# Performance work log

Hardware: AMD Instinct MI355X
Metric: run time of the kernel (lower is better)

Reference implementation:

```python
import jax, jax.numpy as jnp
import numpy as np

EMBED = 1024
HEADS = 16
HEAD_DIM = EMBED // HEADS


def setup_inputs() -> dict:
    key = jax.random.key(0)
    ks = jax.random.split(key, 7)
    N, S = 2, 2048
    k = jax.random.normal(ks[0], (N, S, EMBED), dtype=jnp.float32)
    q = jax.random.normal(ks[1], (N, S, EMBED), dtype=jnp.float32)
    v = jax.random.normal(ks[2], (N, S, EMBED), dtype=jnp.float32)
    sc = 1.0 / np.sqrt(HEAD_DIM)
    # nn.Linear weights, applied as x @ W.T
    Wk = jax.random.normal(ks[3], (HEAD_DIM, HEAD_DIM), dtype=jnp.float32) * sc
    Wq = jax.random.normal(ks[4], (HEAD_DIM, HEAD_DIM), dtype=jnp.float32) * sc
    Wv = jax.random.normal(ks[5], (HEAD_DIM, HEAD_DIM), dtype=jnp.float32) * sc
    Wo = jax.random.normal(ks[6], (EMBED, EMBED), dtype=jnp.float32) / np.sqrt(EMBED)
    return {"k": k, "q": q, "v": v, "Wk": Wk, "Wq": Wq, "Wv": Wv, "Wo": Wo}


def reference(k, q, v, Wk, Wq, Wv, Wo):
    N, S, _ = q.shape
    # reshape to [N, S, H, D]; per-head projection weights shared across heads
    kh = jnp.einsum('nshd,ed->nshe', k.reshape(N, S, HEADS, HEAD_DIM), Wk)
    qh = jnp.einsum('nshd,ed->nshe', q.reshape(N, S, HEADS, HEAD_DIM), Wq)
    vh = jnp.einsum('nshd,ed->nshe', v.reshape(N, S, HEADS, HEAD_DIM), Wv)
    # energy: [N, H, q_len, k_len]
    energy = jnp.einsum('nqhd,nkhd->nhqk', qh, kh)
    attn = jax.nn.softmax(energy / jnp.sqrt(jnp.float32(HEAD_DIM)), axis=-1)
    out = jnp.einsum('nhqk,nkhd->nqhd', attn, vh).reshape(N, S, EMBED)
    return out @ Wo.T
```

## Files before the change

kernel.cpp:

```cpp
#include <hip/hip_runtime.h>

#define SQ   2048
#define HEADS 16
#define HD   64
#define EMB  1024

typedef __attribute__((ext_vector_type(2))) __fp16 h2;
typedef __attribute__((ext_vector_type(4))) __fp16 h4;
typedef __attribute__((ext_vector_type(8))) __fp16 h8;
typedef __attribute__((ext_vector_type(4))) float f4;
typedef unsigned short USH;
typedef unsigned int   UI;

__device__ __forceinline__ UI pkh(float a, float b) {
    h2 v = __builtin_amdgcn_cvt_pkrtz(a, b);
    return __builtin_bit_cast(UI, v);
}

__device__ __forceinline__ void glds16(const void* g, void* l) {
    __builtin_amdgcn_global_load_lds(
        (const __attribute__((address_space(1))) unsigned int*)g,
        (__attribute__((address_space(3))) unsigned int*)l, 16, 0, 0);
}

__global__ __launch_bounds__(256) void proj_fused(
    const float* __restrict__ q_in, const float* __restrict__ k_in,
    const float* __restrict__ v_in, const float* __restrict__ Wq,
    const float* __restrict__ Wk,   const float* __restrict__ Wv,
    const float* __restrict__ Wo,
    USH* __restrict__ Qh, USH* __restrict__ Kh, USH* __restrict__ Vt,
    USH* __restrict__ Wob)
{
    int t = threadIdx.x;
    if (blockIdx.y == 3) {
        int i = blockIdx.x * 256 + t;
        for (int j = 0; j < 4; ++j) {
            float4 v = ((const float4*)Wo)[i + j * 65536];
            uint2 pk; pk.x = pkh(v.x, v.y); pk.y = pkh(v.z, v.w);
            *(uint2*)(Wob + ((size_t)i + (size_t)j * 65536) * 4) = pk;
        }
        return;
    }
    const float* X = (blockIdx.y == 0) ? q_in : (blockIdx.y == 1) ? k_in : v_in;
    const float* W = (blockIdx.y == 0) ? Wq   : (blockIdx.y == 1) ? Wk   : Wv;
    float scale    = (blockIdx.y == 0) ? 0.18033688011112043f : 1.0f;

    __shared__ __align__(16) USH Xl[256][72];
    __shared__ __align__(16) USH Wl[64][72];

    const float4* Xg = (const float4*)(X + (size_t)blockIdx.x * 16384);
    for (int j = 0; j < 16; ++j) {
        int f = t + j * 256;
        float4 v = Xg[f];
        int row = f >> 4; int col = (f & 15) << 2;
        uint2 pk; pk.x = pkh(v.x, v.y); pk.y = pkh(v.z, v.w);
        *(uint2*)&Xl[row][col] = pk;
    }
    const float4* Wg = (const float4*)W;
    for (int j = 0; j < 4; ++j) {
        int f = t + j * 256;
        float4 v = Wg[f];
        int row = f >> 4; int col = (f & 15) << 2;
        uint2 pk; pk.x = pkh(v.x, v.y); pk.y = pkh(v.z, v.w);
        *(uint2*)&Wl[row][col] = pk;
    }
    __syncthreads();

    int wv = t >> 6, lane = t & 63, l4 = lane & 15, quad = lane >> 4;

    h8 wf[4][2], xf[4][2];
    for (int et = 0; et < 4; ++et)
        for (int ks = 0; ks < 2; ++ks)
            wf[et][ks] = *(const h8*)&Wl[et * 16 + l4][ks * 32 + quad * 8];
    for (int rt = 0; rt < 4; ++rt)
        for (int ks = 0; ks < 2; ++ks)
            xf[rt][ks] = *(const h8*)&Xl[wv * 64 + rt * 16 + l4][ks * 32 + quad * 8];

    f4 acc[4][4];
    for (int et = 0; et < 4; ++et)
        for (int rt = 0; rt < 4; ++rt) acc[et][rt] = (f4)(0.0f);
    for (int et = 0; et < 4; ++et)
        for (int rt = 0; rt < 4; ++rt)
            for (int ks = 0; ks < 2; ++ks)
                acc[et][rt] = __builtin_amdgcn_mfma_f32_16x16x32_f16(
                    wf[et][ks], xf[rt][ks], acc[et][rt], 0, 0, 0);

    if (blockIdx.y == 2) {
        int ns0 = blockIdx.x * 16 + wv * 4;
        int n = ns0 >> 11, s = ns0 & 2047;
        for (int et = 0; et < 4; ++et)
            for (int j = 0; j < 4; ++j) {
                int e = et * 16 + quad * 4 + j;
                uint2 pk;
                pk.x = pkh(acc[et][0][j], acc[et][1][j]);
                pk.y = pkh(acc[et][2][j], acc[et][3][j]);
                *(uint2*)(Vt + (((size_t)(n * HEADS + l4) * HD + e) * SQ + s)) = pk;
            }
    } else {
        USH* Out = (blockIdx.y == 0) ? Qh : Kh;
        for (int rt = 0; rt < 4; ++rt) {
            int ns = blockIdx.x * 16 + wv * 4 + rt;
            int n = ns >> 11, s = ns & 2047;
            USH* ob = Out + (((size_t)(n * HEADS) + l4) * SQ + s) * HD;
            for (int et = 0; et < 4; ++et) {
                uint2 pk;
                pk.x = pkh(acc[et][rt][0] * scale, acc[et][rt][1] * scale);
                pk.y = pkh(acc[et][rt][2] * scale, acc[et][rt][3] * scale);
                *(uint2*)(ob + et * 16 + quad * 4) = pk;
            }
        }
    }
}

__device__ __forceinline__ void stage_kv(const USH* __restrict__ Kg,
                                         const USH* __restrict__ Vg,
                                         int kt, USH* Kd, USH* Vd,
                                         int w, int lane)
{
#pragma unroll
    for (int j = 0; j < 2; ++j) {
        int s = (w * 2 + j) * 64 + lane;
        int r = s >> 3, c = (s & 7) ^ (r & 7);
        glds16(Kg + kt * 4096 + r * 64 + c * 8, Kd + s * 8);
    }
#pragma unroll
    for (int j = 0; j < 2; ++j) {
        int s = (w * 2 + j) * 64 + lane;
        int r = s >> 3, c = (s & 7) ^ (r & 7);
        glds16(Vg + r * SQ + kt * 64 + c * 8, Vd + s * 8);
    }
}

__global__ __launch_bounds__(256, 3) void attn_kernel(
    const USH* __restrict__ Qh, const USH* __restrict__ Kh,
    const USH* __restrict__ Vt, USH* __restrict__ Oh)
{
    __shared__ union {
        struct { USH K[2][4096]; USH V[2][4096]; } s;
        struct { float Osum[64][68]; float Lsum[64]; } r;
    } lds;

    int t = threadIdx.x, w = t >> 6, lane = t & 63;
    int l4 = lane & 15, quad = lane >> 4;
    int b = blockIdx.x;
    int nh = b & 31;
    int q0 = (b >> 5) * 64;
    const USH* Qg = Qh + ((size_t)nh * SQ + q0) * HD;
    const USH* Kg = Kh + (size_t)nh * SQ * HD;
    const USH* Vg = Vt + (size_t)nh * HD * SQ;

    h8 bq[4][2];
#pragma unroll
    for (int qt = 0; qt < 4; ++qt)
#pragma unroll
        for (int ks = 0; ks < 2; ++ks)
            bq[qt][ks] = *(const h8*)(Qg + (size_t)(qt * 16 + l4) * HD + ks * 32 + quad * 8);

    f4 o[4][4];
#pragma unroll
    for (int dt = 0; dt < 4; ++dt)
#pragma unroll
        for (int qt = 0; qt < 4; ++qt) o[dt][qt] = (f4)(0.0f);
    float lsum[4] = {0.f, 0.f, 0.f, 0.f};

    int key = w * 16 + l4;
    int kslot0 = key * 8 + (quad ^ (key & 7));
    int kslot1 = key * 8 + ((4 + quad) ^ (key & 7));
    int dchunk = w * 2 + (quad >> 1);
    int vbyte  = (quad & 1) * 4;

    stage_kv(Kg, Vg, 0, lds.s.K[0], lds.s.V[0], w, lane);

    for (int kt = 0; kt < SQ / 64; ++kt) {
        int cur = kt & 1;
        __syncthreads();
        if (kt + 1 < SQ / 64)
            stage_kv(Kg, Vg, kt + 1, lds.s.K[cur ^ 1], lds.s.V[cur ^ 1], w, lane);

        h8 ak0 = *(const h8*)(lds.s.K[cur] + kslot0 * 8);
        h8 ak1 = *(const h8*)(lds.s.K[cur] + kslot1 * 8);

        f4 sc[4];
#pragma unroll
        for (int qt = 0; qt < 4; ++qt) {
            f4 s0 = __builtin_amdgcn_mfma_f32_16x16x32_f16(ak0, bq[qt][0], (f4)(0.0f), 0, 0, 0);
            sc[qt] = __builtin_amdgcn_mfma_f32_16x16x32_f16(ak1, bq[qt][1], s0, 0, 0, 0);
        }

        h4 av[4];
#pragma unroll
        for (int dt = 0; dt < 4; ++dt) {
            int d = dt * 16 + l4;
            int vs = d * 8 + (dchunk ^ (d & 7));
            av[dt] = *(const h4*)(lds.s.V[cur] + vs * 8 + vbyte);
        }

        h4 p[4];
#pragma unroll
        for (int qt = 0; qt < 4; ++qt) {
            float p0 = __builtin_amdgcn_exp2f(sc[qt][0]);
            float p1 = __builtin_amdgcn_exp2f(sc[qt][1]);
            float p2 = __builtin_amdgcn_exp2f(sc[qt][2]);
            float p3 = __builtin_amdgcn_exp2f(sc[qt][3]);
            lsum[qt] += (p0 + p1) + (p2 + p3);
            uint2 u; u.x = pkh(p0, p1); u.y = pkh(p2, p3);
            p[qt] = __builtin_bit_cast(h4, u);
        }

#pragma unroll
        for (int dt = 0; dt < 4; ++dt)
#pragma unroll
            for (int qt = 0; qt < 4; ++qt)
                o[dt][qt] = __builtin_amdgcn_mfma_f32_16x16x16f16(
                    av[dt], p[qt], o[dt][qt], 0, 0, 0);
    }

#pragma unroll
    for (int qt = 0; qt < 4; ++qt) {
        lsum[qt] += __shfl_xor(lsum[qt], 16, 64);
        lsum[qt] += __shfl_xor(lsum[qt], 32, 64);
    }

    __syncthreads();
    for (int ph = 0; ph < 4; ++ph) {
        if (w == ph) {
            for (int dt = 0; dt < 4; ++dt)
                for (int qt = 0; qt < 4; ++qt) {
                    float* dst = &lds.r.Osum[qt * 16 + l4][dt * 16 + quad * 4];
                    f4 val = o[dt][qt];
                    if (ph) val += *(const f4*)dst;
                    *(f4*)dst = val;
                }
            if (quad == 0)
                for (int qt = 0; qt < 4; ++qt) {
                    int qi = qt * 16 + l4;
                    lds.r.Lsum[qi] = ph ? (lds.r.Lsum[qi] + lsum[qt]) : lsum[qt];
                }
        }
        __syncthreads();
    }

    int n = nh >> 4, h = nh & 15;
    int q = t >> 2, d0 = (t & 3) * 16;
    float inv = 1.0f / lds.r.Lsum[q];
    float vv[16];
#pragma unroll
    for (int i = 0; i < 4; ++i) {
        f4 x = *(const f4*)&lds.r.Osum[q][d0 + i * 4];
        vv[i * 4 + 0] = x[0] * inv; vv[i * 4 + 1] = x[1] * inv;
        vv[i * 4 + 2] = x[2] * inv; vv[i * 4 + 3] = x[3] * inv;
    }
    uint4 ou0, ou1;
    ou0.x = pkh(vv[0], vv[1]);   ou0.y = pkh(vv[2], vv[3]);
    ou0.z = pkh(vv[4], vv[5]);   ou0.w = pkh(vv[6], vv[7]);
    ou1.x = pkh(vv[8], vv[9]);   ou1.y = pkh(vv[10], vv[11]);
    ou1.z = pkh(vv[12], vv[13]); ou1.w = pkh(vv[14], vv[15]);
    USH* ob = Oh + ((size_t)(n * SQ + q0 + q)) * EMB + h * HD + d0;
    *(uint4*)ob = ou0;
    *(uint4*)(ob + 8) = ou1;
}

__global__ __launch_bounds__(256, 4) void gemm_bt(const USH* __restrict__ A,
                                                  const USH* __restrict__ B,
                                                  float* __restrict__ C)
{
    __shared__ __align__(16) USH Al[2][4096];
    __shared__ __align__(16) USH Bl[2][4096];
    int t = threadIdx.x, w = t >> 6, lane = t & 63;
    int l4 = lane & 15, quad = lane >> 4;
    int b = blockIdx.x;
    int m0 = (b & 63) * 64;
    int n0 = (b >> 6) * 64;
    int wm = (w >> 1) * 32, wn = (w & 1) * 32;

    f4 acc[2][2];
    for (int mt = 0; mt < 2; ++mt)
        for (int nt = 0; nt < 2; ++nt) acc[mt][nt] = (f4)(0.0f);

    int aslot[2][2], bslot[2][2];
#pragma unroll
    for (int mt = 0; mt < 2; ++mt)
#pragma unroll
        for (int ks = 0; ks < 2; ++ks) {
            int m = wm + mt * 16 + l4;
            aslot[mt][ks] = m * 8 + ((ks * 4 + quad) ^ (m & 7));
            int nn = wn + mt * 16 + l4;
            bslot[mt][ks] = nn * 8 + ((ks * 4 + quad) ^ (nn & 7));
        }

#pragma unroll
    for (int j = 0; j < 2; ++j) {
        int s = (w * 2 + j) * 64 + lane;
        int r = s >> 3, c = (s & 7) ^ (r & 7);
        glds16(A + (size_t)(m0 + r) * 1024 + c * 8, Al[0] + s * 8);
        glds16(B + (size_t)(n0 + r) * 1024 + c * 8, Bl[0] + s * 8);
    }

    for (int ki = 0; ki < 16; ++ki) {
        int cur = ki & 1;
        __syncthreads();
        if (ki + 1 < 16) {
            int k0 = (ki + 1) * 64;
#pragma unroll
            for (int j = 0; j < 2; ++j) {
                int s = (w * 2 + j) * 64 + lane;
                int r = s >> 3, c = (s & 7) ^ (r & 7);
                glds16(A + (size_t)(m0 + r) * 1024 + k0 + c * 8, Al[cur ^ 1] + s * 8);
                glds16(B + (size_t)(n0 + r) * 1024 + k0 + c * 8, Bl[cur ^ 1] + s * 8);
            }
        }

        h8 a[2][2], bf[2][2];
#pragma unroll
        for (int mt = 0; mt < 2; ++mt)
#pragma unroll
            for (int ks = 0; ks < 2; ++ks) {
                a[mt][ks]  = *(const h8*)(Al[cur] + aslot[mt][ks] * 8);
                bf[mt][ks] = *(const h8*)(Bl[cur] + bslot[mt][ks] * 8);
            }
#pragma unroll
        for (int mt = 0; mt < 2; ++mt)
#pragma unroll
            for (int nt = 0; nt < 2; ++nt)
#pragma unroll
                for (int ks = 0; ks < 2; ++ks)
                    acc[mt][nt] = __builtin_amdgcn_mfma_f32_16x16x32_f16(
                        a[mt][ks], bf[nt][ks], acc[mt][nt], 0, 0, 0);
    }

    for (int mt = 0; mt < 2; ++mt)
        for (int nt = 0; nt < 2; ++nt)
            for (int r = 0; r < 4; ++r)
                C[(size_t)(m0 + wm + mt * 16 + quad * 4 + r) * 1024 +
                  (n0 + wn + nt * 16 + l4)] = acc[mt][nt][r];
}

extern "C" void kernel_launch(void* const* d_in, const int* in_sizes, int n_in,
                              void* d_out, int out_size, void* d_ws, size_t ws_size,
                              hipStream_t stream) {
    const float* k_in = (const float*)d_in[0];
    const float* q_in = (const float*)d_in[1];
    const float* v_in = (const float*)d_in[2];
    const float* Wk   = (const float*)d_in[3];
    const float* Wq   = (const float*)d_in[4];
    const float* Wv   = (const float*)d_in[5];
    const float* Wo   = (const float*)d_in[6];
    float* out = (float*)d_out;

    char* ws = (char*)d_ws;
    USH* Qh  = (USH*)(ws);
    USH* Kh  = (USH*)(ws + 8388608);
    USH* Vt  = (USH*)(ws + 16777216);
    USH* Oh  = (USH*)(ws + 25165824);
    USH* Wob = (USH*)(ws + 33554432);

    proj_fused<<<dim3(256, 4), dim3(256), 0, stream>>>(
        q_in, k_in, v_in, Wq, Wk, Wv, Wo, Qh, Kh, Vt, Wob);
    attn_kernel<<<dim3(1024), dim3(256), 0, stream>>>(Qh, Kh, Vt, Oh);
    gemm_bt<<<dim3(1024), dim3(256), 0, stream>>>(Oh, Wob, out);
}
```

Before: 186.2 us.

## Give each wave private K/V LDS buffers and drop per-tile block barriers

Each wave now stages only its own 16-key slice of K and V into a private double-buffered LDS region, so the per-iteration __syncthreads is replaced by a wave-local vmcnt wait. LDS reads for the current tile are issued before the next tile's async global-to-LDS loads, with sched_barriers to fix the ordering. The LDS swizzle changes to match the smaller per-wave tiles. This removes block-wide synchronization stalls but relies on the waitcnt encoding and on intra-wave ordering being correct for the async loads.

```diff
diff --git a/kernel.cpp b/kernel.cpp
--- a/kernel.cpp
+++ b/kernel.cpp
@@ -112,31 +112,12 @@
     }
 }
 
-__device__ __forceinline__ void stage_kv(const USH* __restrict__ Kg,
-                                         const USH* __restrict__ Vg,
-                                         int kt, USH* Kd, USH* Vd,
-                                         int w, int lane)
-{
-#pragma unroll
-    for (int j = 0; j < 2; ++j) {
-        int s = (w * 2 + j) * 64 + lane;
-        int r = s >> 3, c = (s & 7) ^ (r & 7);
-        glds16(Kg + kt * 4096 + r * 64 + c * 8, Kd + s * 8);
-    }
-#pragma unroll
-    for (int j = 0; j < 2; ++j) {
-        int s = (w * 2 + j) * 64 + lane;
-        int r = s >> 3, c = (s & 7) ^ (r & 7);
-        glds16(Vg + r * SQ + kt * 64 + c * 8, Vd + s * 8);
-    }
-}
-
 __global__ __launch_bounds__(256, 3) void attn_kernel(
     const USH* __restrict__ Qh, const USH* __restrict__ Kh,
     const USH* __restrict__ Vt, USH* __restrict__ Oh)
 {
     __shared__ union {
-        struct { USH K[2][4096]; USH V[2][4096]; } s;
+        struct { USH K[4][2][1024]; USH V[4][2][1024]; } s;
         struct { float Osum[64][68]; float Lsum[64]; } r;
     } lds;
 
@@ -146,8 +127,8 @@
     int nh = b & 31;
     int q0 = (b >> 5) * 64;
     const USH* Qg = Qh + ((size_t)nh * SQ + q0) * HD;
-    const USH* Kg = Kh + (size_t)nh * SQ * HD;
-    const USH* Vg = Vt + (size_t)nh * HD * SQ;
+    const USH* Kg = Kh + ((size_t)nh * SQ + (size_t)w * 16) * HD;
+    const USH* Vg = Vt + (size_t)nh * HD * SQ + w * 16;
 
     h8 bq[4][2];
 #pragma unroll
@@ -163,36 +144,60 @@
         for (int qt = 0; qt < 4; ++qt) o[dt][qt] = (f4)(0.0f);
     float lsum[4] = {0.f, 0.f, 0.f, 0.f};
 
-    int key = w * 16 + l4;
-    int kslot0 = key * 8 + (quad ^ (key & 7));
-    int kslot1 = key * 8 + ((4 + quad) ^ (key & 7));
-    int dchunk = w * 2 + (quad >> 1);
-    int vbyte  = (quad & 1) * 4;
-
-    stage_kv(Kg, Vg, 0, lds.s.K[0], lds.s.V[0], w, lane);
-
+    int ksr[2], ksc[2], vsr[2], vsc[2];
+#pragma unroll
+    for (int j = 0; j < 2; ++j) {
+        int s = j * 64 + lane;
+        ksr[j] = s >> 3; ksc[j] = (s & 7) ^ (ksr[j] & 7);
+        vsr[j] = s >> 1; vsc[j] = (s & 1) ^ (vsr[j] & 1);
+    }
+    int kslot0 = l4 * 8 + ((0 * 4 + quad) ^ (l4 & 7));
+    int kslot1 = l4 * 8 + ((1 * 4 + quad) ^ (l4 & 7));
+    int vhalf  = (quad & 1) * 4;
+
+    USH* Kd[2] = { lds.s.K[w][0], lds.s.K[w][1] };
+    USH* Vd[2] = { lds.s.V[w][0], lds.s.V[w][1] };
+
+#pragma unroll
+    for (int j = 0; j < 2; ++j)
+        glds16(Kg + (size_t)ksr[j] * HD + ksc[j] * 8, Kd[0] + (j * 64 + lane) * 8);
+#pragma unroll
+    for (int j = 0; j < 2; ++j)
+        glds16(Vg + (size_t)vsr[j] * SQ + vsc[j] * 8, Vd[0] + (j * 64 + lane) * 8);
+
+#pragma unroll 1
     for (int kt = 0; kt < SQ / 64; ++kt) {
         int cur = kt & 1;
-        __syncthreads();
-        if (kt + 1 < SQ / 64)
-            stage_kv(Kg, Vg, kt + 1, lds.s.K[cur ^ 1], lds.s.V[cur ^ 1], w, lane);
-
-        h8 ak0 = *(const h8*)(lds.s.K[cur] + kslot0 * 8);
-        h8 ak1 = *(const h8*)(lds.s.K[cur] + kslot1 * 8);
+        __builtin_amdgcn_s_waitcnt(0x0F70);
+        __builtin_amdgcn_sched_barrier(0);
+
+        h8 ak0 = *(const h8*)(Kd[cur] + kslot0 * 8);
+        h8 ak1 = *(const h8*)(Kd[cur] + kslot1 * 8);
+        h4 av[4];
+#pragma unroll
+        for (int dt = 0; dt < 4; ++dt) {
+            int d = dt * 16 + l4;
+            int vs = d * 2 + ((quad >> 1) ^ (d & 1));
+            av[dt] = *(const h4*)(Vd[cur] + vs * 8 + vhalf);
+        }
+        __builtin_amdgcn_sched_barrier(0);
+
+        if (kt + 1 < SQ / 64) {
+            const USH* kg = Kg + (size_t)(kt + 1) * 64 * HD;
+            const USH* vg = Vg + (kt + 1) * 64;
+#pragma unroll
+            for (int j = 0; j < 2; ++j)
+                glds16(kg + (size_t)ksr[j] * HD + ksc[j] * 8, Kd[cur ^ 1] + (j * 64 + lane) * 8);
+#pragma unroll
+            for (int j = 0; j < 2; ++j)
+                glds16(vg + (size_t)vsr[j] * SQ + vsc[j] * 8, Vd[cur ^ 1] + (j * 64 + lane) * 8);
+        }
 
         f4 sc[4];
 #pragma unroll
         for (int qt = 0; qt < 4; ++qt) {
             f4 s0 = __builtin_amdgcn_mfma_f32_16x16x32_f16(ak0, bq[qt][0], (f4)(0.0f), 0, 0, 0);
             sc[qt] = __builtin_amdgcn_mfma_f32_16x16x32_f16(ak1, bq[qt][1], s0, 0, 0, 0);
-        }
-
-        h4 av[4];
-#pragma unroll
-        for (int dt = 0; dt < 4; ++dt) {
-            int d = dt * 16 + l4;
-            int vs = d * 8 + (dchunk ^ (d & 7));
-            av[dt] = *(const h4*)(lds.s.V[cur] + vs * 8 + vbyte);
         }
 
         h4 p[4];
```

Measured after the change: 187.3 us. Within noise of the previous version (+0.6%).
